# Kernel tuning notes

Hardware: AMD Instinct MI355X
Metric: run time of the kernel (lower is better)

## Reference

```python
import jax, jax.numpy as jnp
import numpy as np

N_NODES = 10000
N_EDGES = 100000
MUL = 32        # multiplicity of 0e and 1o in node feats / out irreps
ATTR = 16       # node_attrs scalars
RADIAL = 8      # edge_feats scalars
W_NUMEL = 4 * MUL * MUL  # 4 CG paths, fully-connected [mul1=32, mul2=1, mul_out=32]


def setup_inputs() -> dict:
    key = jax.random.key(0)
    ks = jax.random.split(key, 12)
    return {
        'node_attrs': jax.random.normal(ks[0], (N_NODES, ATTR), jnp.float32),
        'node_feats': jax.random.normal(ks[1], (N_NODES, 4 * MUL), jnp.float32),  # 32x0e | 32x1o flattened
        'edge_attrs': jax.random.normal(ks[2], (N_EDGES, 4), jnp.float32),        # Y0 | Y1 (3 comps)
        'edge_feats': jax.random.normal(ks[3], (N_EDGES, RADIAL), jnp.float32),
        'edge_index': jax.random.randint(ks[4], (2, N_EDGES), 0, N_NODES, jnp.int32),
        'Wgen': jax.random.normal(ks[5], (RADIAL, W_NUMEL), jnp.float32),  # conv_tp_weights (o3.Linear on scalars)
        'L1s': jax.random.normal(ks[6], (MUL, MUL), jnp.float32),  # linear_1, scalar block
        'L1v': jax.random.normal(ks[7], (MUL, MUL), jnp.float32),  # linear_1, vector block
        'WS0': jax.random.normal(ks[8], (MUL, ATTR, MUL), jnp.float32),  # skip_tp 0e*0e->0e
        'WS1': jax.random.normal(ks[9], (MUL, ATTR, MUL), jnp.float32),  # skip_tp 1o*0e->1o
        'L2s': jax.random.normal(ks[10], (MUL, MUL), jnp.float32),
        'L2v': jax.random.normal(ks[11], (MUL, MUL), jnp.float32),
    }


def reference(node_attrs, node_feats, edge_attrs, edge_feats, edge_index,
              Wgen, L1s, L1v, WS0, WS1, L2s, L2v):
    sender, receiver = edge_index[0], edge_index[1]
    n = node_attrs.shape[0]

    # gather sender node feats, split irreps: [E,32] scalars, [E,32,3] vectors
    g = node_feats[sender]
    xs = g[:, :MUL]
    xv = g[:, MUL:].reshape(-1, MUL, 3)
    ys = edge_attrs[:, 0]    # l=0 edge attr
    yv = edge_attrs[:, 1:]   # l=1 edge attr, [E,3]

    # per-edge generated tensor-product weights (o3.Linear on scalar edge feats)
    tw = (edge_feats @ Wgen) * (1.0 / np.sqrt(RADIAL))
    tw = tw.reshape(-1, 4, MUL, MUL)
    WA, WB, WC, WD = tw[:, 0], tw[:, 1], tw[:, 2], tw[:, 3]

    # fully-connected CG tensor product (4 paths, edge attrs have mul=1)
    outA = jnp.einsum('euw,eu,e->ew', WA, xs, ys)          # 0e x 0e -> 0e
    outB = jnp.einsum('euw,eu,ei->ewi', WB, xs, yv)        # 0e x 1o -> 1o
    outC = jnp.einsum('euw,eui,e->ewi', WC, xv, ys)        # 1o x 0e -> 1o
    dot = jnp.einsum('eui,ei->eu', xv, yv) * (1.0 / np.sqrt(3.0))  # CG for 1o x 1o -> 0e
    outD = jnp.einsum('euw,eu->ew', WD, dot)
    alpha = 1.0 / np.sqrt(2 * MUL)  # fan-in path normalization (2 paths x mul1=32 per output irrep)
    ms = (outA + outD) * alpha      # [E,32]
    mv = (outB + outC) * alpha      # [E,32,3]

    # linear_1 (per-irrep mixing)
    lnorm = 1.0 / np.sqrt(MUL)
    ms = (ms @ L1s) * lnorm
    mv = jnp.einsum('ewi,wu->eui', mv, L1v) * lnorm

    # scatter-sum messages to receiver nodes
    Ms = jax.ops.segment_sum(ms, receiver, num_segments=n)   # [N,32]
    Mv = jax.ops.segment_sum(mv, receiver, num_segments=n)   # [N,32,3]

    # skip_tp: out irreps x node_attrs (16x0e) -> out irreps
    snorm = 1.0 / np.sqrt(MUL * ATTR)
    ss = jnp.einsum('uvw,nu,nv->nw', WS0, Ms, node_attrs) * snorm
    sv = jnp.einsum('uvw,nui,nv->nwi', WS1, Mv, node_attrs) * snorm

    # linear_2
    ss = (ss @ L2s) * lnorm
    sv = jnp.einsum('nwi,wu->nui', sv, L2v) * lnorm

    # residual, flatten irreps back to [N, 128]
    return jnp.concatenate([Ms + ss, (Mv + sv).reshape(n, 3 * MUL)], axis=1)
```

## Files before the change

### kernel.cpp

```cpp
#include <hip/hip_runtime.h>

#define N_NODES 10000
#define N_EDGES 100000
#define SLOTS 40

typedef __attribute__((ext_vector_type(8))) _Float16 f16x8;
typedef __attribute__((ext_vector_type(2))) _Float16 f16x2;
typedef __attribute__((ext_vector_type(4))) float f32x4;

static __device__ inline f16x2 pkrtz(float a, float b) {
    auto t = __builtin_amdgcn_cvt_pkrtz(a, b);
    union { decltype(t) x; f16x2 y; } u;
    u.x = t;
    return u.y;
}
static __device__ inline unsigned short f16u(float x) {
    union { _Float16 h; unsigned short s; } u;
    u.h = (_Float16)x;
    return u.s;
}
static __device__ inline float f16f(unsigned short us) {
    union { unsigned short s; _Float16 h; } u;
    u.s = us;
    return (float)u.h;
}
static __device__ inline f16x8 cvt8h(const float* f) {
    f16x8 r; f16x2* rp = (f16x2*)&r;
#pragma unroll
    for (int i = 0; i < 4; ++i) rp[i] = pkrtz(f[2 * i], f[2 * i + 1]);
    return r;
}
static __device__ inline f16x8 scale8(f16x2 h2, f16x8 x) {
    f16x8 r; f16x2* rp = (f16x2*)&r; f16x2* xp = (f16x2*)&x;
#pragma unroll
    for (int i = 0; i < 4; ++i) rp[i] = h2 * xp[i];
    return r;
}
static __device__ inline int pack2(float a, float b) {
    union { f16x2 h; int i; } u;
    u.h = pkrtz(a, b);
    return u.i;
}
static __device__ inline f16x8 dot3(f16x8 xx, f16x8 xy, f16x8 xz, f32x4 ea) {
    _Float16 y0 = (_Float16)ea.y, y1 = (_Float16)ea.z, y2 = (_Float16)ea.w;
    f16x2 y0_2 = {y0, y0}, y1_2 = {y1, y1}, y2_2 = {y2, y2};
    f16x8 r; f16x2* rp = (f16x2*)&r;
    f16x2* xp = (f16x2*)&xx; f16x2* yp = (f16x2*)&xy; f16x2* zp = (f16x2*)&xz;
#pragma unroll
    for (int i = 0; i < 4; ++i)
        rp[i] = xp[i] * y0_2 + yp[i] * y1_2 + zp[i] * y2_2;
    return r;
}

__global__ __launch_bounds__(1024) void prep_kernel(
    const float* __restrict__ Wgen, const float* __restrict__ L1s,
    const float* __restrict__ L1v, const float* __restrict__ WS0,
    const float* __restrict__ WS1, const float* __restrict__ L2s,
    const float* __restrict__ L2v, const float* __restrict__ node_feats,
    unsigned short* __restrict__ Wc, unsigned short* __restrict__ WB0,
    unsigned short* __restrict__ WB1, unsigned short* __restrict__ xf,
    int* __restrict__ cnt) {
    const float S = 1.0f / 128.0f;
    int tid = blockIdx.x * 1024 + threadIdx.x;
    if (tid < N_NODES) cnt[tid] = 0;
    if (tid < 40000) {
        int n = tid >> 2, qq = tid & 3;
        const float* g = node_feats + n * 128;
        unsigned short* dst = xf + (size_t)tid * 32;
#pragma unroll
        for (int j = 0; j < 8; ++j) dst[j] = f16u(g[qq * 8 + j]);
#pragma unroll
        for (int c = 0; c < 3; ++c)
#pragma unroll
            for (int j = 0; j < 8; ++j)
                dst[8 + c * 8 + j] = f16u(g[32 + qq * 24 + j * 3 + c]);
    }
    if (tid < 32768) {
        int j = tid & 7;
        int lane = (tid >> 3) & 63;
        int ks = (tid >> 9) & 7;
        int nt = tid >> 12;
        int col = nt * 16 + (lane & 15);
        int u = (lane >> 4) * 8 + j;
        int r = ks;
        int p, c2;
        const float* M;
        float sc = S;
        if (col < 32)      { p = 0; M = L1s; c2 = col; }
        else if (col < 64) { p = 1; M = L1v; c2 = col - 32; }
        else if (col < 96) { p = 2; M = L1v; c2 = col - 64; }
        else               { p = 3; M = L1s; c2 = col - 96; sc = S * 0.57735026918962576f; }
        const float* wg = Wgen + r * 4096 + p * 1024 + u * 32;
        float acc = 0.f;
#pragma unroll
        for (int w = 0; w < 32; ++w) acc += wg[w] * M[w * 32 + c2];
        Wc[tid] = f16u(acc * sc);
    } else {
        int idx = tid - 32768;
        int table = idx >> 14;
        int r14 = idx & 16383;
        int j = r14 & 7;
        int lane = (r14 >> 3) & 63;
        int ks = (r14 >> 9) & 15;
        int k = ks * 32 + (lane >> 4) * 8 + j;
        int u = k >> 4, v = k & 15;
        int w = ((r14 >> 13) & 1) * 16 + (lane & 15);
        const float* WS = table ? WS1 : WS0;
        const float* L2 = table ? L2v : L2s;
        const float* src = WS + u * 512 + v * 32;
        float acc = 0.f;
#pragma unroll
        for (int x = 0; x < 32; ++x) acc += src[x] * L2[x * 32 + w];
        unsigned short val = f16u(acc * S);
        if (table) WB1[r14] = val; else WB0[r14] = val;
    }
}

__global__ __launch_bounds__(256) void edge_kernel(
    const unsigned short* __restrict__ xf, const float* __restrict__ edge_attrs,
    const float* __restrict__ edge_feats, const int* __restrict__ edge_index,
    const unsigned short* __restrict__ Wc, int* __restrict__ cnt,
    unsigned short* __restrict__ Msg) {
    __shared__ f16x8 sW8[4096];
    __shared__ int sSL[4][16];
    __shared__ f32x4 sEA[4][16];
    {
        const f16x8* src = (const f16x8*)Wc;
        for (int i = threadIdx.x; i < 4096; i += 256) sW8[i] = src[i];
    }
    __syncthreads();

    const int lane = threadIdx.x & 63;
    const int m = lane & 15, q = lane >> 4;
    const int wv = threadIdx.x >> 6;
    const int wave = (blockIdx.x * 256 + threadIdx.x) >> 6;
    const int stride = gridDim.x * 4;
    const int NT = N_EDGES / 16;

    int tile = wave;
    if (tile >= NT) return;

    f16x8 xs8, xv8[3], dt8;
    float efC[8];
    f32x4 eaC;
    int slC = 0;

    {
        int e = tile * 16 + m;
        int snd = edge_index[e];
        if (lane < 16) {
            int r = edge_index[N_EDGES + e];
            slC = r * SLOTS + atomicAdd(&cnt[r], 1);
        }
        const f16x8* gx = (const f16x8*)(xf + (size_t)(snd * 4 + q) * 32);
        xs8 = gx[0]; xv8[0] = gx[1]; xv8[1] = gx[2]; xv8[2] = gx[3];
        *(f32x4*)&efC[0] = *(const f32x4*)(edge_feats + e * 8);
        *(f32x4*)&efC[4] = *(const f32x4*)(edge_feats + e * 8 + 4);
        eaC = *(const f32x4*)(edge_attrs + e * 4);
        dt8 = dot3(xv8[0], xv8[1], xv8[2], eaC);
    }
    int snd1 = 0, rcv1 = 0;
    {
        int t1 = tile + stride;
        if (t1 < NT) {
            int e1 = t1 * 16 + m;
            snd1 = edge_index[e1];
            if (lane < 16) rcv1 = edge_index[N_EDGES + e1];
        }
    }

    while (tile < NT) {
        const int tn = tile + stride;
        const bool hasN = tn < NT;
        const int t2 = tile + 2 * stride;
        const bool has2 = t2 < NT;

        if (lane < 16) {
            sSL[wv][lane] = slC;
            sEA[wv][lane] = eaC;
        }

        f16x8 xsN, xvxN, xvyN, xvzN;
        float efN[8];
        f32x4 eaN;
        int slN = 0;
        if (hasN) {
            int en = tn * 16 + m;
            if (lane < 16) slN = rcv1 * SLOTS + atomicAdd(&cnt[rcv1], 1);
            const f16x8* gN = (const f16x8*)(xf + (size_t)(snd1 * 4 + q) * 32);
            xsN = gN[0]; xvxN = gN[1]; xvyN = gN[2]; xvzN = gN[3];
            *(f32x4*)&efN[0] = *(const f32x4*)(edge_feats + en * 8);
            *(f32x4*)&efN[4] = *(const f32x4*)(edge_feats + en * 8 + 4);
            eaN = *(const f32x4*)(edge_attrs + en * 4);
        }

        int snd2 = 0, rcv2 = 0;
        if (has2) {
            int e2 = t2 * 16 + m;
            snd2 = edge_index[e2];
            if (lane < 16) rcv2 = edge_index[N_EDGES + e2];
        }

        f32x4 z = {0.f, 0.f, 0.f, 0.f};
        f32x4 fA[2] = {z, z}, fB[2] = {z, z}, fD[2] = {z, z};
        f32x4 fC[3][2] = {{z, z}, {z, z}, {z, z}};

#pragma unroll
        for (int ks = 0; ks < 8; ++ks) {
            _Float16 h = (_Float16)efC[ks];
            f16x2 h2 = {h, h};
            {
                f16x8 a = scale8(h2, xs8);
                fA[0] = __builtin_amdgcn_mfma_f32_16x16x32_f16(a, sW8[(0 * 8 + ks) * 64 + lane], fA[0], 0, 0, 0);
                fA[1] = __builtin_amdgcn_mfma_f32_16x16x32_f16(a, sW8[(1 * 8 + ks) * 64 + lane], fA[1], 0, 0, 0);
                fB[0] = __builtin_amdgcn_mfma_f32_16x16x32_f16(a, sW8[(2 * 8 + ks) * 64 + lane], fB[0], 0, 0, 0);
                fB[1] = __builtin_amdgcn_mfma_f32_16x16x32_f16(a, sW8[(3 * 8 + ks) * 64 + lane], fB[1], 0, 0, 0);
            }
            {
                f16x8 bc0 = sW8[(4 * 8 + ks) * 64 + lane];
                f16x8 bc1 = sW8[(5 * 8 + ks) * 64 + lane];
#pragma unroll
                for (int c = 0; c < 3; ++c) {
                    f16x8 a = scale8(h2, xv8[c]);
                    fC[c][0] = __builtin_amdgcn_mfma_f32_16x16x32_f16(a, bc0, fC[c][0], 0, 0, 0);
                    fC[c][1] = __builtin_amdgcn_mfma_f32_16x16x32_f16(a, bc1, fC[c][1], 0, 0, 0);
                }
            }
            {
                f16x8 a = scale8(h2, dt8);
                fD[0] = __builtin_amdgcn_mfma_f32_16x16x32_f16(a, sW8[(6 * 8 + ks) * 64 + lane], fD[0], 0, 0, 0);
                fD[1] = __builtin_amdgcn_mfma_f32_16x16x32_f16(a, sW8[(7 * 8 + ks) * 64 + lane], fD[1], 0, 0, 0);
            }
        }

        int4 sl4 = *(const int4*)&sSL[wv][q * 4];
        const int slR[4] = {sl4.x, sl4.y, sl4.z, sl4.w};
#pragma unroll
        for (int t4 = 0; t4 < 4; ++t4) {
            f32x4 ea4 = sEA[wv][q * 4 + t4];
            float ysr = ea4.x, y0r = ea4.y, y1r = ea4.z, y2r = ea4.w;
            int dr = slR[t4];
#pragma unroll
            for (int nt = 0; nt < 2; ++nt) {
                int col = nt * 16 + m;
                float pb = fB[nt][t4];
                int2 pk;
                pk.x = pack2(ysr * fA[nt][t4] + fD[nt][t4],
                             y0r * pb + ysr * fC[0][nt][t4]);
                pk.y = pack2(y1r * pb + ysr * fC[1][nt][t4],
                             y2r * pb + ysr * fC[2][nt][t4]);
                *(int2*)(Msg + (size_t)dr * 128 + col * 4) = pk;
            }
        }

        tile = tn;
        if (hasN) {
            xs8 = xsN; xv8[0] = xvxN; xv8[1] = xvyN; xv8[2] = xvzN;
            dt8 = dot3(xvxN, xvyN, xvzN, eaN);
#pragma unroll
            for (int j = 0; j < 8; ++j) efC[j] = efN[j];
            eaC = eaN;
            slC = slN;
            snd1 = snd2;
            rcv1 = rcv2;
        }
    }
}

__global__ __launch_bounds__(256) void node_kernel(
    const float* __restrict__ node_attrs, const unsigned short* __restrict__ Msg,
    const int* __restrict__ cnt, const unsigned short* __restrict__ WB0,
    const unsigned short* __restrict__ WB1, float* __restrict__ out) {
    __shared__ float sM[16][129];
    __shared__ float sAt[16][17];
    int n0 = blockIdx.x * 16;

    int nl = threadIdx.x >> 4;
    int cg = threadIdx.x & 15;
    int n = n0 + nl;
    int deg = cnt[n];
    int s0 = n * SLOTS;
    float acc[8];
#pragma unroll
    for (int j = 0; j < 8; ++j) acc[j] = 0.f;
    {
        f32x4 r[16];
#pragma unroll
        for (int i = 0; i < 16; ++i)
            r[i] = *(const f32x4*)(Msg + (size_t)(s0 + i) * 128 + cg * 8);
#pragma unroll
        for (int i = 0; i < 16; ++i) {
            if (i < deg) {
                const unsigned short* us = (const unsigned short*)&r[i];
#pragma unroll
                for (int j = 0; j < 8; ++j) acc[j] += f16f(us[j]);
            }
        }
    }
    for (int s = s0 + 16; s < s0 + deg; ++s) {
        f32x4 raw = *(const f32x4*)(Msg + (size_t)s * 128 + cg * 8);
        const unsigned short* us = (const unsigned short*)&raw;
#pragma unroll
        for (int j = 0; j < 8; ++j) acc[j] += f16f(us[j]);
    }
#pragma unroll
    for (int j = 0; j < 8; ++j)
        sM[nl][(j & 3) * 32 + cg * 2 + (j >> 2)] = acc[j];
    sAt[nl][cg] = node_attrs[n * 16 + cg];
    __syncthreads();

    int p = threadIdx.x >> 6;
    int lane = threadIdx.x & 63;
    int m = lane & 15, q = lane >> 4;
    const unsigned short* WB = (p == 0) ? WB0 : WB1;
    int chb = p * 32;
    f32x4 z = {0.f, 0.f, 0.f, 0.f};
    f32x4 D0 = z, D1 = z;
#pragma unroll
    for (int ks = 0; ks < 16; ++ks) {
        int kb = ks * 32 + q * 8;
        float t[8];
#pragma unroll
        for (int j = 0; j < 8; ++j) {
            int k = kb + j;
            t[j] = sM[m][chb + (k >> 4)] * sAt[m][k & 15];
        }
        f16x8 a = cvt8h(t);
        f16x8 b0 = *(const f16x8*)(WB + (ks * 64 + lane) * 8);
        f16x8 b1 = *(const f16x8*)(WB + ((16 + ks) * 64 + lane) * 8);
        D0 = __builtin_amdgcn_mfma_f32_16x16x32_f16(a, b0, D0, 0, 0, 0);
        D1 = __builtin_amdgcn_mfma_f32_16x16x32_f16(a, b1, D1, 0, 0, 0);
    }

#pragma unroll
    for (int t4 = 0; t4 < 4; ++t4) {
        int nl2 = q * 4 + t4;
        int nn = n0 + nl2;
        if (p == 0) {
            out[nn * 128 + m]      = sM[nl2][m] + D0[t4];
            out[nn * 128 + 16 + m] = sM[nl2][16 + m] + D1[t4];
        } else {
            int i = p - 1;
            out[nn * 128 + 32 + m * 3 + i]        = sM[nl2][chb + m] + D0[t4];
            out[nn * 128 + 32 + (16 + m) * 3 + i] = sM[nl2][chb + 16 + m] + D1[t4];
        }
    }
}

extern "C" void kernel_launch(void* const* d_in, const int* in_sizes, int n_in,
                              void* d_out, int out_size, void* d_ws, size_t ws_size,
                              hipStream_t stream) {
    (void)in_sizes; (void)n_in; (void)out_size; (void)ws_size;
    const float* node_attrs = (const float*)d_in[0];
    const float* node_feats = (const float*)d_in[1];
    const float* edge_attrs = (const float*)d_in[2];
    const float* edge_feats = (const float*)d_in[3];
    const int*   edge_index = (const int*)d_in[4];
    const float* Wgen = (const float*)d_in[5];
    const float* L1s  = (const float*)d_in[6];
    const float* L1v  = (const float*)d_in[7];
    const float* WS0  = (const float*)d_in[8];
    const float* WS1  = (const float*)d_in[9];
    const float* L2s  = (const float*)d_in[10];
    const float* L2v  = (const float*)d_in[11];
    float* out = (float*)d_out;
    char* ws = (char*)d_ws;

    unsigned short* Msg = (unsigned short*)ws;
    unsigned short* Wc  = (unsigned short*)(ws + 102400000);
    unsigned short* WB0 = (unsigned short*)(ws + 102465536);
    unsigned short* WB1 = (unsigned short*)(ws + 102498304);
    int* cnt = (int*)(ws + 102531072);
    unsigned short* xf  = (unsigned short*)(ws + 102571072);

    prep_kernel<<<64, 1024, 0, stream>>>(Wgen, L1s, L1v, WS0, WS1, L2s, L2v,
                                         node_feats, Wc, WB0, WB1, xf, cnt);
    edge_kernel<<<512, 256, 0, stream>>>(xf, edge_attrs, edge_feats,
                                         edge_index, Wc, cnt, Msg);
    node_kernel<<<625, 256, 0, stream>>>(node_attrs, Msg, cnt, WB0, WB1, out);
}
```

Before: 129.7 us.

## Split edge work into scalar/vector block groups and build receiver lists in prep

Edge messages are now written densely, indexed by edge id instead of receiver slot. The receiver bucketing (atomic count plus an edge-id list) moves into the prep kernel, and the node kernel gathers messages through that list. The edge kernel grid is doubled and split 3:5 into blocks that compute only the scalar paths (A,D) or only the vector paths (B,C). This halves each block's shared weight footprint and register pressure, which should raise occupancy. The cost is an extra indirection in the node gather and scattered 2-byte stores for the message output.

```diff
diff --git a/kernel.cpp b/kernel.cpp
--- a/kernel.cpp
+++ b/kernel.cpp
@@ -36,11 +36,6 @@
     for (int i = 0; i < 4; ++i) rp[i] = h2 * xp[i];
     return r;
 }
-static __device__ inline int pack2(float a, float b) {
-    union { f16x2 h; int i; } u;
-    u.h = pkrtz(a, b);
-    return u.i;
-}
 static __device__ inline f16x8 dot3(f16x8 xx, f16x8 xy, f16x8 xz, f32x4 ea) {
     _Float16 y0 = (_Float16)ea.y, y1 = (_Float16)ea.z, y2 = (_Float16)ea.w;
     f16x2 y0_2 = {y0, y0}, y1_2 = {y1, y1}, y2_2 = {y2, y2};
@@ -57,12 +52,17 @@
     const float* __restrict__ L1v, const float* __restrict__ WS0,
     const float* __restrict__ WS1, const float* __restrict__ L2s,
     const float* __restrict__ L2v, const float* __restrict__ node_feats,
-    unsigned short* __restrict__ Wc, unsigned short* __restrict__ WB0,
-    unsigned short* __restrict__ WB1, unsigned short* __restrict__ xf,
-    int* __restrict__ cnt) {
+    const int* __restrict__ edge_index, unsigned short* __restrict__ Wc,
+    unsigned short* __restrict__ WB0, unsigned short* __restrict__ WB1,
+    unsigned short* __restrict__ xf, int* __restrict__ cnt,
+    int* __restrict__ elist) {
     const float S = 1.0f / 128.0f;
     int tid = blockIdx.x * 1024 + threadIdx.x;
-    if (tid < N_NODES) cnt[tid] = 0;
+    for (int e = tid; e < N_EDGES; e += 65536) {
+        int r = edge_index[N_EDGES + e];
+        int k = atomicAdd(&cnt[r], 1);
+        elist[r * SLOTS + k] = e;
+    }
     if (tid < 40000) {
         int n = tid >> 2, qq = tid & 3;
         const float* g = node_feats + n * 128;
@@ -119,106 +119,157 @@
 __global__ __launch_bounds__(256) void edge_kernel(
     const unsigned short* __restrict__ xf, const float* __restrict__ edge_attrs,
     const float* __restrict__ edge_feats, const int* __restrict__ edge_index,
-    const unsigned short* __restrict__ Wc, int* __restrict__ cnt,
-    unsigned short* __restrict__ Msg) {
-    __shared__ f16x8 sW8[4096];
-    __shared__ int sSL[4][16];
+    const unsigned short* __restrict__ Wc, unsigned short* __restrict__ Msg) {
+    __shared__ f16x8 sW[2048];
     __shared__ f32x4 sEA[4][16];
+
+    const int bid = blockIdx.x;
+    const bool h0 = (bid & 7) < 3;
     {
+        int g0, g1, g2, g3;
+        if (h0) { g0 = 0; g1 = 1; g2 = 6; g3 = 7; }
+        else    { g0 = 2; g1 = 3; g2 = 4; g3 = 5; }
         const f16x8* src = (const f16x8*)Wc;
-        for (int i = threadIdx.x; i < 4096; i += 256) sW8[i] = src[i];
+        for (int i = threadIdx.x; i < 2048; i += 256) {
+            int slot = i >> 9, rem = i & 511;
+            int gt = slot == 0 ? g0 : slot == 1 ? g1 : slot == 2 ? g2 : g3;
+            sW[i] = src[(gt << 9) + rem];
+        }
     }
     __syncthreads();
 
     const int lane = threadIdx.x & 63;
     const int m = lane & 15, q = lane >> 4;
     const int wv = threadIdx.x >> 6;
-    const int wave = (blockIdx.x * 256 + threadIdx.x) >> 6;
-    const int stride = gridDim.x * 4;
     const int NT = N_EDGES / 16;
-
-    int tile = wave;
+    const int rank = h0 ? ((bid >> 3) * 3 + (bid & 7))
+                        : ((bid >> 3) * 5 + ((bid & 7) - 3));
+    const int nblk = h0 ? 384 : 640;
+    const int stride = nblk * 4;
+    int tile = rank * 4 + wv;
     if (tile >= NT) return;
 
-    f16x8 xs8, xv8[3], dt8;
     float efC[8];
     f32x4 eaC;
-    int slC = 0;
-
-    {
-        int e = tile * 16 + m;
-        int snd = edge_index[e];
-        if (lane < 16) {
-            int r = edge_index[N_EDGES + e];
-            slC = r * SLOTS + atomicAdd(&cnt[r], 1);
-        }
-        const f16x8* gx = (const f16x8*)(xf + (size_t)(snd * 4 + q) * 32);
-        xs8 = gx[0]; xv8[0] = gx[1]; xv8[1] = gx[2]; xv8[2] = gx[3];
-        *(f32x4*)&efC[0] = *(const f32x4*)(edge_feats + e * 8);
-        *(f32x4*)&efC[4] = *(const f32x4*)(edge_feats + e * 8 + 4);
-        eaC = *(const f32x4*)(edge_attrs + e * 4);
-        dt8 = dot3(xv8[0], xv8[1], xv8[2], eaC);
-    }
-    int snd1 = 0, rcv1 = 0;
-    {
-        int t1 = tile + stride;
-        if (t1 < NT) {
-            int e1 = t1 * 16 + m;
-            snd1 = edge_index[e1];
-            if (lane < 16) rcv1 = edge_index[N_EDGES + e1];
-        }
-    }
-
-    while (tile < NT) {
-        const int tn = tile + stride;
-        const bool hasN = tn < NT;
-        const int t2 = tile + 2 * stride;
-        const bool has2 = t2 < NT;
-
-        if (lane < 16) {
-            sSL[wv][lane] = slC;
-            sEA[wv][lane] = eaC;
-        }
-
-        f16x8 xsN, xvxN, xvyN, xvzN;
-        float efN[8];
-        f32x4 eaN;
-        int slN = 0;
-        if (hasN) {
-            int en = tn * 16 + m;
-            if (lane < 16) slN = rcv1 * SLOTS + atomicAdd(&cnt[rcv1], 1);
-            const f16x8* gN = (const f16x8*)(xf + (size_t)(snd1 * 4 + q) * 32);
-            xsN = gN[0]; xvxN = gN[1]; xvyN = gN[2]; xvzN = gN[3];
-            *(f32x4*)&efN[0] = *(const f32x4*)(edge_feats + en * 8);
-            *(f32x4*)&efN[4] = *(const f32x4*)(edge_feats + en * 8 + 4);
-            eaN = *(const f32x4*)(edge_attrs + en * 4);
-        }
-
-        int snd2 = 0, rcv2 = 0;
-        if (has2) {
-            int e2 = t2 * 16 + m;
-            snd2 = edge_index[e2];
-            if (lane < 16) rcv2 = edge_index[N_EDGES + e2];
-        }
-
-        f32x4 z = {0.f, 0.f, 0.f, 0.f};
-        f32x4 fA[2] = {z, z}, fB[2] = {z, z}, fD[2] = {z, z};
-        f32x4 fC[3][2] = {{z, z}, {z, z}, {z, z}};
-
-#pragma unroll
-        for (int ks = 0; ks < 8; ++ks) {
-            _Float16 h = (_Float16)efC[ks];
-            f16x2 h2 = {h, h};
-            {
-                f16x8 a = scale8(h2, xs8);
-                fA[0] = __builtin_amdgcn_mfma_f32_16x16x32_f16(a, sW8[(0 * 8 + ks) * 64 + lane], fA[0], 0, 0, 0);
-                fA[1] = __builtin_amdgcn_mfma_f32_16x16x32_f16(a, sW8[(1 * 8 + ks) * 64 + lane], fA[1], 0, 0, 0);
-                fB[0] = __builtin_amdgcn_mfma_f32_16x16x32_f16(a, sW8[(2 * 8 + ks) * 64 + lane], fB[0], 0, 0, 0);
-                fB[1] = __builtin_amdgcn_mfma_f32_16x16x32_f16(a, sW8[(3 * 8 + ks) * 64 + lane], fB[1], 0, 0, 0);
-            }
-            {
-                f16x8 bc0 = sW8[(4 * 8 + ks) * 64 + lane];
-                f16x8 bc1 = sW8[(5 * 8 + ks) * 64 + lane];
+
+    if (h0) {
+        f16x8 xs8, dt8;
+        {
+            int e = tile * 16 + m;
+            int snd = edge_index[e];
+            eaC = *(const f32x4*)(edge_attrs + e * 4);
+            const f16x8* gx = (const f16x8*)(xf + (size_t)(snd * 4 + q) * 32);
+            xs8 = gx[0];
+            dt8 = dot3(gx[1], gx[2], gx[3], eaC);
+            *(f32x4*)&efC[0] = *(const f32x4*)(edge_feats + e * 8);
+            *(f32x4*)&efC[4] = *(const f32x4*)(edge_feats + e * 8 + 4);
+        }
+        int snd1 = 0;
+        {
+            int t1 = tile + stride;
+            if (t1 < NT) snd1 = edge_index[t1 * 16 + m];
+        }
+        while (tile < NT) {
+            const int tn = tile + stride;
+            const bool hasN = tn < NT;
+            const int t2 = tile + 2 * stride;
+
+            if (lane < 16) sEA[wv][lane] = eaC;
+
+            f16x8 xsN, xvxN, xvyN, xvzN;
+            float efN[8];
+            f32x4 eaN;
+            if (hasN) {
+                int en = tn * 16 + m;
+                const f16x8* gN = (const f16x8*)(xf + (size_t)(snd1 * 4 + q) * 32);
+                xsN = gN[0]; xvxN = gN[1]; xvyN = gN[2]; xvzN = gN[3];
+                *(f32x4*)&efN[0] = *(const f32x4*)(edge_feats + en * 8);
+                *(f32x4*)&efN[4] = *(const f32x4*)(edge_feats + en * 8 + 4);
+                eaN = *(const f32x4*)(edge_attrs + en * 4);
+            }
+            int snd2 = 0;
+            if (t2 < NT) snd2 = edge_index[t2 * 16 + m];
+
+            f32x4 z = {0.f, 0.f, 0.f, 0.f};
+            f32x4 fA[2] = {z, z}, fD[2] = {z, z};
+#pragma unroll
+            for (int ks = 0; ks < 8; ++ks) {
+                _Float16 h = (_Float16)efC[ks];
+                f16x2 h2 = {h, h};
+                f16x8 aS = scale8(h2, xs8);
+                fA[0] = __builtin_amdgcn_mfma_f32_16x16x32_f16(aS, sW[(0 * 8 + ks) * 64 + lane], fA[0], 0, 0, 0);
+                fA[1] = __builtin_amdgcn_mfma_f32_16x16x32_f16(aS, sW[(1 * 8 + ks) * 64 + lane], fA[1], 0, 0, 0);
+                f16x8 aD = scale8(h2, dt8);
+                fD[0] = __builtin_amdgcn_mfma_f32_16x16x32_f16(aD, sW[(2 * 8 + ks) * 64 + lane], fD[0], 0, 0, 0);
+                fD[1] = __builtin_amdgcn_mfma_f32_16x16x32_f16(aD, sW[(3 * 8 + ks) * 64 + lane], fD[1], 0, 0, 0);
+            }
+#pragma unroll
+            for (int t4 = 0; t4 < 4; ++t4) {
+                float ysr = sEA[wv][q * 4 + t4].x;
+                size_t row = (size_t)(tile * 16 + q * 4 + t4) * 128;
+#pragma unroll
+                for (int nt = 0; nt < 2; ++nt)
+                    Msg[row + nt * 16 + m] = f16u(ysr * fA[nt][t4] + fD[nt][t4]);
+            }
+            tile = tn;
+            if (hasN) {
+                xs8 = xsN;
+                dt8 = dot3(xvxN, xvyN, xvzN, eaN);
+#pragma unroll
+                for (int j = 0; j < 8; ++j) efC[j] = efN[j];
+                eaC = eaN;
+                snd1 = snd2;
+            }
+        }
+    } else {
+        f16x8 xs8, xv8[3];
+        {
+            int e = tile * 16 + m;
+            int snd = edge_index[e];
+            eaC = *(const f32x4*)(edge_attrs + e * 4);
+            const f16x8* gx = (const f16x8*)(xf + (size_t)(snd * 4 + q) * 32);
+            xs8 = gx[0]; xv8[0] = gx[1]; xv8[1] = gx[2]; xv8[2] = gx[3];
+            *(f32x4*)&efC[0] = *(const f32x4*)(edge_feats + e * 8);
+            *(f32x4*)&efC[4] = *(const f32x4*)(edge_feats + e * 8 + 4);
+        }
+        int snd1 = 0;
+        {
+            int t1 = tile + stride;
+            if (t1 < NT) snd1 = edge_index[t1 * 16 + m];
+        }
+        while (tile < NT) {
+            const int tn = tile + stride;
+            const bool hasN = tn < NT;
+            const int t2 = tile + 2 * stride;
+
+            if (lane < 16) sEA[wv][lane] = eaC;
+
+            f16x8 xsN, xvxN, xvyN, xvzN;
+            float efN[8];
+            f32x4 eaN;
+            if (hasN) {
+                int en = tn * 16 + m;
+                const f16x8* gN = (const f16x8*)(xf + (size_t)(snd1 * 4 + q) * 32);
+                xsN = gN[0]; xvxN = gN[1]; xvyN = gN[2]; xvzN = gN[3];
+                *(f32x4*)&efN[0] = *(const f32x4*)(edge_feats + en * 8);
+                *(f32x4*)&efN[4] = *(const f32x4*)(edge_feats + en * 8 + 4);
+                eaN = *(const f32x4*)(edge_attrs + en * 4);
+            }
+            int snd2 = 0;
+            if (t2 < NT) snd2 = edge_index[t2 * 16 + m];
+
+            f32x4 z = {0.f, 0.f, 0.f, 0.f};
+            f32x4 fB[2] = {z, z};
+            f32x4 fC[3][2] = {{z, z}, {z, z}, {z, z}};
+#pragma unroll
+            for (int ks = 0; ks < 8; ++ks) {
+                _Float16 h = (_Float16)efC[ks];
+                f16x2 h2 = {h, h};
+                f16x8 aS = scale8(h2, xs8);
+                fB[0] = __builtin_amdgcn_mfma_f32_16x16x32_f16(aS, sW[(0 * 8 + ks) * 64 + lane], fB[0], 0, 0, 0);
+                fB[1] = __builtin_amdgcn_mfma_f32_16x16x32_f16(aS, sW[(1 * 8 + ks) * 64 + lane], fB[1], 0, 0, 0);
+                f16x8 bc0 = sW[(2 * 8 + ks) * 64 + lane];
+                f16x8 bc1 = sW[(3 * 8 + ks) * 64 + lane];
 #pragma unroll
                 for (int c = 0; c < 3; ++c) {
                     f16x8 a = scale8(h2, xv8[c]);
@@ -226,51 +277,38 @@
                     fC[c][1] = __builtin_amdgcn_mfma_f32_16x16x32_f16(a, bc1, fC[c][1], 0, 0, 0);
                 }
             }
-            {
-                f16x8 a = scale8(h2, dt8);
-                fD[0] = __builtin_amdgcn_mfma_f32_16x16x32_f16(a, sW8[(6 * 8 + ks) * 64 + lane], fD[0], 0, 0, 0);
-                fD[1] = __builtin_amdgcn_mfma_f32_16x16x32_f16(a, sW8[(7 * 8 + ks) * 64 + lane], fD[1], 0, 0, 0);
-            }
-        }
-
-        int4 sl4 = *(const int4*)&sSL[wv][q * 4];
-        const int slR[4] = {sl4.x, sl4.y, sl4.z, sl4.w};
-#pragma unroll
-        for (int t4 = 0; t4 < 4; ++t4) {
-            f32x4 ea4 = sEA[wv][q * 4 + t4];
-            float ysr = ea4.x, y0r = ea4.y, y1r = ea4.z, y2r = ea4.w;
-            int dr = slR[t4];
-#pragma unroll
-            for (int nt = 0; nt < 2; ++nt) {
-                int col = nt * 16 + m;
-                float pb = fB[nt][t4];
-                int2 pk;
-                pk.x = pack2(ysr * fA[nt][t4] + fD[nt][t4],
-                             y0r * pb + ysr * fC[0][nt][t4]);
-                pk.y = pack2(y1r * pb + ysr * fC[1][nt][t4],
-                             y2r * pb + ysr * fC[2][nt][t4]);
-                *(int2*)(Msg + (size_t)dr * 128 + col * 4) = pk;
-            }
-        }
-
-        tile = tn;
-        if (hasN) {
-            xs8 = xsN; xv8[0] = xvxN; xv8[1] = xvyN; xv8[2] = xvzN;
-            dt8 = dot3(xvxN, xvyN, xvzN, eaN);
-#pragma unroll
-            for (int j = 0; j < 8; ++j) efC[j] = efN[j];
-            eaC = eaN;
-            slC = slN;
-            snd1 = snd2;
-            rcv1 = rcv2;
+#pragma unroll
+            for (int t4 = 0; t4 < 4; ++t4) {
+                f32x4 ea4 = sEA[wv][q * 4 + t4];
+                float ysr = ea4.x;
+                float yr[3] = {ea4.y, ea4.z, ea4.w};
+                size_t row = (size_t)(tile * 16 + q * 4 + t4) * 128;
+#pragma unroll
+                for (int nt = 0; nt < 2; ++nt) {
+                    float pb = fB[nt][t4];
+#pragma unroll
+                    for (int c = 0; c < 3; ++c)
+                        Msg[row + 32 + c * 32 + nt * 16 + m] =
+                            f16u(yr[c] * pb + ysr * fC[c][nt][t4]);
+                }
+            }
+            tile = tn;
+            if (hasN) {
+                xs8 = xsN; xv8[0] = xvxN; xv8[1] = xvyN; xv8[2] = xvzN;
+#pragma unroll
+                for (int j = 0; j < 8; ++j) efC[j] = efN[j];
+                eaC = eaN;
+                snd1 = snd2;
+            }
         }
     }
 }
 
 __global__ __launch_bounds__(256) void node_kernel(
     const float* __restrict__ node_attrs, const unsigned short* __restrict__ Msg,
-    const int* __restrict__ cnt, const unsigned short* __restrict__ WB0,
-    const unsigned short* __restrict__ WB1, float* __restrict__ out) {
+    const int* __restrict__ cnt, const int* __restrict__ elist,
+    const unsigned short* __restrict__ WB0, const unsigned short* __restrict__ WB1,
+    float* __restrict__ out) {
     __shared__ float sM[16][129];
     __shared__ float sAt[16][17];
     int n0 = blockIdx.x * 16;
@@ -279,15 +317,21 @@
     int cg = threadIdx.x & 15;
     int n = n0 + nl;
     int deg = cnt[n];
-    int s0 = n * SLOTS;
+    const int* el = elist + n * SLOTS;
     float acc[8];
 #pragma unroll
     for (int j = 0; j < 8; ++j) acc[j] = 0.f;
     {
+        int4 e4[4];
+#pragma unroll
+        for (int i = 0; i < 4; ++i) e4[i] = *(const int4*)(el + i * 4);
+        const int* ei = (const int*)e4;
         f32x4 r[16];
 #pragma unroll
-        for (int i = 0; i < 16; ++i)
-            r[i] = *(const f32x4*)(Msg + (size_t)(s0 + i) * 128 + cg * 8);
+        for (int i = 0; i < 16; ++i) {
+            int e = (i < deg) ? ei[i] : 0;
+            r[i] = *(const f32x4*)(Msg + (size_t)e * 128 + cg * 8);
+        }
 #pragma unroll
         for (int i = 0; i < 16; ++i) {
             if (i < deg) {
@@ -297,15 +341,15 @@
             }
         }
     }
-    for (int s = s0 + 16; s < s0 + deg; ++s) {
-        f32x4 raw = *(const f32x4*)(Msg + (size_t)s * 128 + cg * 8);
+    for (int s = 16; s < deg; ++s) {
+        int e = el[s];
+        f32x4 raw = *(const f32x4*)(Msg + (size_t)e * 128 + cg * 8);
         const unsigned short* us = (const unsigned short*)&raw;
 #pragma unroll
         for (int j = 0; j < 8; ++j) acc[j] += f16f(us[j]);
     }
 #pragma unroll
-    for (int j = 0; j < 8; ++j)
-        sM[nl][(j & 3) * 32 + cg * 2 + (j >> 2)] = acc[j];
+    for (int j = 0; j < 8; ++j) sM[nl][cg * 8 + j] = acc[j];
     sAt[nl][cg] = node_attrs[n * 16 + cg];
     __syncthreads();
 
@@ -367,15 +411,19 @@
     char* ws = (char*)d_ws;
 
     unsigned short* Msg = (unsigned short*)ws;
-    unsigned short* Wc  = (unsigned short*)(ws + 102400000);
-    unsigned short* WB0 = (unsigned short*)(ws + 102465536);
-    unsigned short* WB1 = (unsigned short*)(ws + 102498304);
-    int* cnt = (int*)(ws + 102531072);
-    unsigned short* xf  = (unsigned short*)(ws + 102571072);
-
+    unsigned short* Wc  = (unsigned short*)(ws + 25600000);
+    unsigned short* WB0 = (unsigned short*)(ws + 25665536);
+    unsigned short* WB1 = (unsigned short*)(ws + 25698304);
+    int* cnt   = (int*)(ws + 25731072);
+    int* elist = (int*)(ws + 25771072);
+    unsigned short* xf = (unsigned short*)(ws + 27371072);
+
+    hipMemsetAsync(cnt, 0, N_NODES * sizeof(int), stream);
     prep_kernel<<<64, 1024, 0, stream>>>(Wgen, L1s, L1v, WS0, WS1, L2s, L2v,
-                                         node_feats, Wc, WB0, WB1, xf, cnt);
-    edge_kernel<<<512, 256, 0, stream>>>(xf, edge_attrs, edge_feats,
-                                         edge_index, Wc, cnt, Msg);
-    node_kernel<<<625, 256, 0, stream>>>(node_attrs, Msg, cnt, WB0, WB1, out);
-}
+                                         node_feats, edge_index, Wc, WB0, WB1,
+                                         xf, cnt, elist);
+    edge_kernel<<<1024, 256, 0, stream>>>(xf, edge_attrs, edge_feats,
+                                          edge_index, Wc, Msg);
+    node_kernel<<<625, 256, 0, stream>>>(node_attrs, Msg, cnt, elist,
+                                         WB0, WB1, out);
+}
```

Measured after the change: 136.3 us. +5.1%, slower.

## Store messages per edge densely and gather via per-node edge index lists

Applied to the files above, without the earlier changes.

The edge kernel previously wrote each message into a per-receiver slot region (N_NODES*SLOTS rows), scattering writes across a 100MB buffer. Now messages are written contiguously by edge id into a 25.6MB buffer, and only the edge id is recorded in a per-node slot list. The node kernel reads the index list, then gathers the message rows by edge id. This shrinks the workspace footprint and makes the edge-side writes coalesced, at the cost of an extra indirection and random-row gathers on the node side.

```diff
diff --git a/kernel.cpp b/kernel.cpp
--- a/kernel.cpp
+++ b/kernel.cpp
@@ -120,9 +120,8 @@
     const unsigned short* __restrict__ xf, const float* __restrict__ edge_attrs,
     const float* __restrict__ edge_feats, const int* __restrict__ edge_index,
     const unsigned short* __restrict__ Wc, int* __restrict__ cnt,
-    unsigned short* __restrict__ Msg) {
+    int* __restrict__ elist, unsigned short* __restrict__ Msg) {
     __shared__ f16x8 sW8[4096];
-    __shared__ int sSL[4][16];
     __shared__ f32x4 sEA[4][16];
     {
         const f16x8* src = (const f16x8*)Wc;
@@ -143,14 +142,14 @@
     f16x8 xs8, xv8[3], dt8;
     float efC[8];
     f32x4 eaC;
-    int slC = 0;
 
     {
         int e = tile * 16 + m;
         int snd = edge_index[e];
         if (lane < 16) {
             int r = edge_index[N_EDGES + e];
-            slC = r * SLOTS + atomicAdd(&cnt[r], 1);
+            int k = atomicAdd(&cnt[r], 1);
+            elist[r * SLOTS + k] = e;
         }
         const f16x8* gx = (const f16x8*)(xf + (size_t)(snd * 4 + q) * 32);
         xs8 = gx[0]; xv8[0] = gx[1]; xv8[1] = gx[2]; xv8[2] = gx[3];
@@ -159,34 +158,29 @@
         eaC = *(const f32x4*)(edge_attrs + e * 4);
         dt8 = dot3(xv8[0], xv8[1], xv8[2], eaC);
     }
-    int snd1 = 0, rcv1 = 0;
+    int snd1 = 0;
     {
         int t1 = tile + stride;
-        if (t1 < NT) {
-            int e1 = t1 * 16 + m;
-            snd1 = edge_index[e1];
-            if (lane < 16) rcv1 = edge_index[N_EDGES + e1];
-        }
+        if (t1 < NT) snd1 = edge_index[t1 * 16 + m];
     }
 
     while (tile < NT) {
         const int tn = tile + stride;
         const bool hasN = tn < NT;
         const int t2 = tile + 2 * stride;
-        const bool has2 = t2 < NT;
-
-        if (lane < 16) {
-            sSL[wv][lane] = slC;
-            sEA[wv][lane] = eaC;
-        }
+
+        if (lane < 16) sEA[wv][lane] = eaC;
 
         f16x8 xsN, xvxN, xvyN, xvzN;
         float efN[8];
         f32x4 eaN;
-        int slN = 0;
         if (hasN) {
             int en = tn * 16 + m;
-            if (lane < 16) slN = rcv1 * SLOTS + atomicAdd(&cnt[rcv1], 1);
+            if (lane < 16) {
+                int r = edge_index[N_EDGES + en];
+                int k = atomicAdd(&cnt[r], 1);
+                elist[r * SLOTS + k] = en;
+            }
             const f16x8* gN = (const f16x8*)(xf + (size_t)(snd1 * 4 + q) * 32);
             xsN = gN[0]; xvxN = gN[1]; xvyN = gN[2]; xvzN = gN[3];
             *(f32x4*)&efN[0] = *(const f32x4*)(edge_feats + en * 8);
@@ -194,12 +188,8 @@
             eaN = *(const f32x4*)(edge_attrs + en * 4);
         }
 
-        int snd2 = 0, rcv2 = 0;
-        if (has2) {
-            int e2 = t2 * 16 + m;
-            snd2 = edge_index[e2];
-            if (lane < 16) rcv2 = edge_index[N_EDGES + e2];
-        }
+        int snd2 = 0;
+        if (t2 < NT) snd2 = edge_index[t2 * 16 + m];
 
         f32x4 z = {0.f, 0.f, 0.f, 0.f};
         f32x4 fA[2] = {z, z}, fB[2] = {z, z}, fD[2] = {z, z};
@@ -233,13 +223,11 @@
             }
         }
 
-        int4 sl4 = *(const int4*)&sSL[wv][q * 4];
-        const int slR[4] = {sl4.x, sl4.y, sl4.z, sl4.w};
 #pragma unroll
         for (int t4 = 0; t4 < 4; ++t4) {
             f32x4 ea4 = sEA[wv][q * 4 + t4];
             float ysr = ea4.x, y0r = ea4.y, y1r = ea4.z, y2r = ea4.w;
-            int dr = slR[t4];
+            size_t row = (size_t)(tile * 16 + q * 4 + t4) * 128;
 #pragma unroll
             for (int nt = 0; nt < 2; ++nt) {
                 int col = nt * 16 + m;
@@ -249,7 +237,7 @@
                              y0r * pb + ysr * fC[0][nt][t4]);
                 pk.y = pack2(y1r * pb + ysr * fC[1][nt][t4],
                              y2r * pb + ysr * fC[2][nt][t4]);
-                *(int2*)(Msg + (size_t)dr * 128 + col * 4) = pk;
+                *(int2*)(Msg + row + col * 4) = pk;
             }
         }
 
@@ -260,17 +248,16 @@
 #pragma unroll
             for (int j = 0; j < 8; ++j) efC[j] = efN[j];
             eaC = eaN;
-            slC = slN;
             snd1 = snd2;
-            rcv1 = rcv2;
         }
     }
 }
 
 __global__ __launch_bounds__(256) void node_kernel(
     const float* __restrict__ node_attrs, const unsigned short* __restrict__ Msg,
-    const int* __restrict__ cnt, const unsigned short* __restrict__ WB0,
-    const unsigned short* __restrict__ WB1, float* __restrict__ out) {
+    const int* __restrict__ cnt, const int* __restrict__ elist,
+    const unsigned short* __restrict__ WB0, const unsigned short* __restrict__ WB1,
+    float* __restrict__ out) {
     __shared__ float sM[16][129];
     __shared__ float sAt[16][17];
     int n0 = blockIdx.x * 16;
@@ -279,15 +266,21 @@
     int cg = threadIdx.x & 15;
     int n = n0 + nl;
     int deg = cnt[n];
-    int s0 = n * SLOTS;
+    const int* el = elist + n * SLOTS;
     float acc[8];
 #pragma unroll
     for (int j = 0; j < 8; ++j) acc[j] = 0.f;
     {
+        int4 e4[4];
+#pragma unroll
+        for (int i = 0; i < 4; ++i) e4[i] = *(const int4*)(el + i * 4);
+        const int* ei = (const int*)e4;
         f32x4 r[16];
 #pragma unroll
-        for (int i = 0; i < 16; ++i)
-            r[i] = *(const f32x4*)(Msg + (size_t)(s0 + i) * 128 + cg * 8);
+        for (int i = 0; i < 16; ++i) {
+            int e = (i < deg) ? ei[i] : 0;
+            r[i] = *(const f32x4*)(Msg + (size_t)e * 128 + cg * 8);
+        }
 #pragma unroll
         for (int i = 0; i < 16; ++i) {
             if (i < deg) {
@@ -297,8 +290,9 @@
             }
         }
     }
-    for (int s = s0 + 16; s < s0 + deg; ++s) {
-        f32x4 raw = *(const f32x4*)(Msg + (size_t)s * 128 + cg * 8);
+    for (int s = 16; s < deg; ++s) {
+        int e = el[s];
+        f32x4 raw = *(const f32x4*)(Msg + (size_t)e * 128 + cg * 8);
         const unsigned short* us = (const unsigned short*)&raw;
 #pragma unroll
         for (int j = 0; j < 8; ++j) acc[j] += f16f(us[j]);
@@ -367,15 +361,17 @@
     char* ws = (char*)d_ws;
 
     unsigned short* Msg = (unsigned short*)ws;
-    unsigned short* Wc  = (unsigned short*)(ws + 102400000);
-    unsigned short* WB0 = (unsigned short*)(ws + 102465536);
-    unsigned short* WB1 = (unsigned short*)(ws + 102498304);
-    int* cnt = (int*)(ws + 102531072);
-    unsigned short* xf  = (unsigned short*)(ws + 102571072);
+    unsigned short* Wc  = (unsigned short*)(ws + 25600000);
+    unsigned short* WB0 = (unsigned short*)(ws + 25665536);
+    unsigned short* WB1 = (unsigned short*)(ws + 25698304);
+    int* cnt   = (int*)(ws + 25731072);
+    int* elist = (int*)(ws + 25771072);
+    unsigned short* xf = (unsigned short*)(ws + 27371072);
 
     prep_kernel<<<64, 1024, 0, stream>>>(Wgen, L1s, L1v, WS0, WS1, L2s, L2v,
                                          node_feats, Wc, WB0, WB1, xf, cnt);
     edge_kernel<<<512, 256, 0, stream>>>(xf, edge_attrs, edge_feats,
-                                         edge_index, Wc, cnt, Msg);
-    node_kernel<<<625, 256, 0, stream>>>(node_attrs, Msg, cnt, WB0, WB1, out);
-}
+                                         edge_index, Wc, cnt, elist, Msg);
+    node_kernel<<<625, 256, 0, stream>>>(node_attrs, Msg, cnt, elist,
+                                         WB0, WB1, out);
+}
```

Result: slower. 133.4 us (+2.9%).
